# Performance work log

Hardware: AMD Instinct MI355X
Metric: run time of the kernel (lower is better)

Reference implementation:

```python
import jax, jax.numpy as jnp
import numpy as np

N_ENT = 50000
N_REL = 500
N_EDGE = 640000
D_IN = 128
D_OUT = 128
NEG_SLOPE = 0.01  # torch nn.LeakyReLU default
BN_EPS = 1e-5


def setup_inputs() -> dict:
    key = jax.random.key(0)
    ks = jax.random.split(key, 16)
    edge_index = jax.random.randint(ks[0], (2, N_EDGE), 0, N_ENT)
    edge_type = jax.random.randint(ks[1], (N_EDGE,), 0, N_REL)
    query_type = jax.random.randint(ks[2], (N_EDGE,), 0, N_REL)
    entity_embed = jax.random.normal(ks[3], (N_ENT, D_IN), jnp.float32)
    rel_embed = jax.random.normal(ks[4], (N_REL, D_IN), jnp.float32)
    s = 0.05
    return {
        "edge_index": edge_index,
        "edge_type": edge_type,
        "query_type": query_type,
        "entity_embed": entity_embed,
        "rel_embed": rel_embed,
        "w_loop": jax.random.normal(ks[5], (D_IN, D_OUT), jnp.float32) * s,
        "w_out": jax.random.normal(ks[6], (D_IN, D_OUT), jnp.float32) * s,
        "w_rel": jax.random.normal(ks[7], (D_IN, D_OUT), jnp.float32) * s,
        "loop_rel": jax.random.normal(ks[8], (1, D_IN), jnp.float32) * s,
        "W_w": jax.random.normal(ks[9], (D_IN, D_IN), jnp.float32) * s,   # W.weight^T layout: x @ W_w
        "W_b": jnp.zeros((D_IN,), jnp.float32),
        "a_w": jax.random.normal(ks[10], (2 * D_IN, 1), jnp.float32) * s,
        "a_b": jnp.zeros((1,), jnp.float32),
        "bias": jnp.zeros((D_OUT,), jnp.float32),
        "bn_gamma": jnp.ones((D_OUT,), jnp.float32),
        "bn_beta": jnp.zeros((D_OUT,), jnp.float32),
    }


def _compgcn_fwd(edge_index, edge_type, query_type, entity_embed, rel_embed,
                 w_loop, w_out, w_rel, loop_rel, W_w, W_b, a_w, a_b,
                 bias, bn_gamma, bn_beta):
    N = entity_embed.shape[0]
    rel_all = jnp.concatenate([rel_embed, loop_rel], axis=0)  # (R+1, D)
    row, col = edge_index[0], edge_index[1]  # values already in [0, N)

    # edge norm: 1/out-degree of source node (deg[row] >= 1 for every edge)
    deg = jax.ops.segment_sum(jnp.ones((row.shape[0],), entity_embed.dtype), row, num_segments=N)
    norm = 1.0 / deg[row]  # (E,)

    # self-loop branch (mode='loop'): rel_transform 'mult' with loop relation, no attention
    loop_res = (entity_embed * rel_all[-1]) @ w_loop  # (N, D_out)

    # out branch (mode='out')
    x_j = entity_embed[col]          # (E, D)
    r_e = rel_all[edge_type]         # (E, D)
    q_e = rel_all[query_type]        # (E, D)
    xj_rel = x_j * r_e               # 'mult' composition

    h = jnp.concatenate([r_e @ W_w + W_b, q_e @ W_w + W_b], axis=-1)  # (E, 2D)
    logits = h @ a_w + a_b                                            # (E, 1)
    alpha = jnp.exp(jax.nn.leaky_relu(logits[:, 0], NEG_SLOPE))       # (E,)
    sum_alpha = jax.ops.segment_sum(alpha, row, num_segments=N)       # (N,)
    alpha = alpha / sum_alpha[row]

    msg = (xj_rel @ w_out) * (alpha * norm)[:, None]                  # (E, D_out)
    out_res = jax.ops.segment_sum(msg, row, num_segments=N)           # (N, D_out)

    out = 0.5 * out_res + 0.5 * loop_res + bias  # dropout = identity (eval)
    # BatchNorm1d, training-mode batch statistics (biased var), over node dim
    mean = jnp.mean(out, axis=0)
    var = jnp.mean((out - mean) ** 2, axis=0)
    out = (out - mean) * jax.lax.rsqrt(var + BN_EPS) * bn_gamma + bn_beta

    ent_out = jax.nn.leaky_relu(out, NEG_SLOPE)
    rel_out = (rel_all @ w_rel)[:-1]
    return ent_out, rel_out


def reference(edge_index, edge_type, query_type, entity_embed, rel_embed,
              w_loop, w_out, w_rel, loop_rel, W_w, W_b, a_w, a_b,
              bias, bn_gamma, bn_beta):
    return _compgcn_fwd(edge_index, edge_type, query_type, entity_embed, rel_embed,
                        w_loop, w_out, w_rel, loop_rel, W_w, W_b, a_w, a_b,
                        bias, bn_gamma, bn_beta)
```

## Files before the change

### kernel.cpp

```cpp
#include <hip/hip_runtime.h>
#include <math.h>

#define E_N 640000
#define N_N 50000
#define R_N 500
#define D   128
#define NEG 0.01f
#define BNEPS 1e-5f
#define CAP 48

typedef __bf16 bf16x8 __attribute__((ext_vector_type(8)));
typedef float f32x4 __attribute__((ext_vector_type(4)));

#define CNT_OFF    0u
#define STAT_OFF   50000u
#define ZERO_FLOATS 50256u
#define BUCKET_OFF 50256u
#define ENTBF_OFF  4850256u
#define RELBF_OFF  8050256u
#define BT_OFF     8082256u
#define S1_OFF     8098640u
#define S2_OFF     8099152u

__device__ __forceinline__ float lrelu(float x) { return x > 0.f ? x : NEG * x; }

__device__ __forceinline__ void st_bf16x4(__bf16* p, float x, float y, float z, float w) {
    union { __bf16 b[4]; uint2 u; } pk;
    pk.b[0] = (__bf16)x; pk.b[1] = (__bf16)y; pk.b[2] = (__bf16)z; pk.b[3] = (__bf16)w;
    *(uint2*)p = pk.u;
}

__device__ __forceinline__ void st_bf16x8(__bf16* p, const float* v) {
    union { __bf16 b[8]; uint4 u; } pk;
#pragma unroll
    for (int j = 0; j < 8; ++j) pk.b[j] = (__bf16)v[j];
    *(uint4*)p = pk.u;
}

__device__ __forceinline__ void fma8(uint4 ue, uint4 ur, float a, float* acc) {
    const unsigned* we = (const unsigned*)&ue;
    const unsigned* wr = (const unsigned*)&ur;
#pragma unroll
    for (int w = 0; w < 4; ++w) {
        float e_lo = __uint_as_float(we[w] << 16);
        float e_hi = __uint_as_float(we[w] & 0xffff0000u);
        float r_lo = __uint_as_float(wr[w] << 16);
        float r_hi = __uint_as_float(wr[w] & 0xffff0000u);
        acc[2 * w]     = fmaf(a * e_lo, r_lo, acc[2 * w]);
        acc[2 * w + 1] = fmaf(a * e_hi, r_hi, acc[2 * w + 1]);
    }
}

#define P1_S   501
#define P1_WB  256
#define P1_REL 500

__global__ __launch_bounds__(128) void k_pre1(const float* __restrict__ Ww,
                                              const float* __restrict__ Wb,
                                              const float* __restrict__ aw,
                                              const float* __restrict__ rel,
                                              const float* __restrict__ looprel,
                                              const float* __restrict__ wout,
                                              const float* __restrict__ wloop,
                                              const float* __restrict__ wrel,
                                              float* __restrict__ s1,
                                              float* __restrict__ s2,
                                              __bf16* __restrict__ Bt,
                                              float* __restrict__ out_rel,
                                              __bf16* __restrict__ rel_bf) {
    int b = blockIdx.x, t = threadIdx.x;
    if (b < P1_S) {
        __shared__ float rr[D];
        __shared__ float part[4];
        const float* rp = (b < R_N) ? rel + (size_t)b * D : looprel;
        rr[t] = rp[t];
        if (b < R_N) rel_bf[(size_t)b * D + t] = (__bf16)rp[t];
        __syncthreads();
        float v = 0.f;
        for (int i = 0; i < D; ++i) v = fmaf(rr[i], Ww[i * D + t], v);
        float p1 = aw[t] * v + Wb[t] * aw[t];
        float p2 = aw[D + t] * v + Wb[t] * aw[D + t];
        for (int o = 32; o; o >>= 1) {
            p1 += __shfl_down(p1, o);
            p2 += __shfl_down(p2, o);
        }
        if ((t & 63) == 0) {
            part[(t >> 6) * 2] = p1;
            part[(t >> 6) * 2 + 1] = p2;
        }
        __syncthreads();
        if (t == 0) {
            s1[b] = part[0] + part[2];
            s2[b] = part[1] + part[3];
        }
    } else if (b < P1_S + P1_WB) {
        int idx = (b - P1_S) * 128 + t;
        int n = idx & 127, k = idx >> 7;
        float v = (k < D) ? wout[(size_t)k * D + n] : wloop[(size_t)(k - D) * D + n];
        Bt[(size_t)n * 256 + k] = (__bf16)v;
    } else {
        int r = b - (P1_S + P1_WB);
        __shared__ float rr2[D];
        rr2[t] = rel[(size_t)r * D + t];
        __syncthreads();
        float a = 0.f;
        for (int k = 0; k < D; ++k) a = fmaf(rr2[k], wrel[(size_t)k * D + t], a);
        out_rel[(size_t)r * D + t] = a;
    }
}

#define P2_BIN 625
#define P2_ENT 1563

__global__ __launch_bounds__(256) void k_pre2(const int* __restrict__ row,
                                              const int* __restrict__ col,
                                              const int* __restrict__ et,
                                              const int* __restrict__ qt,
                                              const float* __restrict__ s1,
                                              const float* __restrict__ s2,
                                              const float* __restrict__ ab,
                                              const float* __restrict__ ent,
                                              int* __restrict__ cnt,
                                              int2* __restrict__ bucket,
                                              __bf16* __restrict__ ent_bf) {
    int b = blockIdx.x, t = threadIdx.x;
    if (b < P2_BIN) {
        int e0 = b * 1024 + t;
        int r[4], c[4], te[4];
        float a[4];
#pragma unroll
        for (int j = 0; j < 4; ++j) {
            int e = e0 + j * 256;
            r[j] = row[e];
            c[j] = col[e];
            te[j] = et[e];
            int q = qt[e];
            a[j] = __expf(lrelu(s1[te[j]] + s2[q] + ab[0]));
        }
        int pos[4];
#pragma unroll
        for (int j = 0; j < 4; ++j) pos[j] = atomicAdd(&cnt[r[j]], 1);
#pragma unroll
        for (int j = 0; j < 4; ++j) {
            if (pos[j] < CAP) {
                bucket[(size_t)r[j] * CAP + pos[j]] =
                    make_int2(c[j] | (te[j] << 16), __float_as_int(a[j]));
            }
        }
    } else {
        int blk = b - P2_BIN;
        const float4* e4 = (const float4*)ent;
#pragma unroll
        for (int j = 0; j < 4; ++j) {
            int idx = blk * 1024 + j * 256 + t;
            if (idx < N_N * D / 4) {
                float4 v = e4[idx];
                st_bf16x4(ent_bf + (size_t)idx * 4, v.x, v.y, v.z, v.w);
            }
        }
    }
}

__global__ __launch_bounds__(128) void k_gather(const int* __restrict__ cnt,
                                                const int2* __restrict__ bucket,
                                                const __bf16* __restrict__ ent_bf,
                                                const __bf16* __restrict__ rel_bf,
                                                const float* __restrict__ looprel,
                                                __bf16* __restrict__ stage) {
    int n = blockIdx.x, t = threadIdx.x;
    int deg = cnt[n];
    int m = deg < CAP ? deg : CAP;
    __shared__ int eoff[CAP];
    __shared__ int roff[CAP];
    __shared__ float sa[CAP];
    __shared__ float xred[16][8];
    if (t < CAP) {
        if (t < m) {
            int2 be = bucket[(size_t)n * CAP + t];
            eoff[t] = (be.x & 0xffff) << 8;
            roff[t] = (be.x >> 16) << 8;
            sa[t] = __int_as_float(be.y);
        } else {
            eoff[t] = 0; roff[t] = 0; sa[t] = 0.f;
        }
    }
    __syncthreads();
    float suma = 0.f;
    for (int i = 0; i < m; ++i) suma += sa[i];
    int s = t & 15, g = t >> 4;
    const char* eb = (const char*)ent_bf;
    const char* rb = (const char*)rel_bf;
    int co = s * 16;
    float acc[8] = {0, 0, 0, 0, 0, 0, 0, 0};
#define EDGE(e_) { \
        uint4 ue = *(const uint4*)(eb + (eoff[e_] + co)); \
        uint4 ur = *(const uint4*)(rb + (roff[e_] + co)); \
        fma8(ue, ur, sa[e_], acc); }
    EDGE(g) EDGE(g + 8)
    if (m > 16) { EDGE(g + 16) EDGE(g + 24) }
    if (m > 32) { EDGE(g + 32) EDGE(g + 40) }
#undef EDGE
#pragma unroll
    for (int k = 0; k < 8; ++k) {
        acc[k] += __shfl_xor(acc[k], 16);
        acc[k] += __shfl_xor(acc[k], 32);
    }
    if (t >= 64 && t < 80) {
#pragma unroll
        for (int k = 0; k < 8; ++k) xred[s][k] = acc[k];
    }
    if (t >= 96 && t < 112) {
        int si = t - 96;
        uint4 ue = *(const uint4*)(eb + ((size_t)n << 8) + si * 16);
        const unsigned* we = (const unsigned*)&ue;
        float v[8];
#pragma unroll
        for (int w = 0; w < 4; ++w) {
            v[2 * w]     = __uint_as_float(we[w] << 16) * looprel[si * 8 + 2 * w];
            v[2 * w + 1] = __uint_as_float(we[w] & 0xffff0000u) * looprel[si * 8 + 2 * w + 1];
        }
        st_bf16x8(stage + (size_t)n * 256 + 128 + si * 8, v);
    }
    __syncthreads();
    if (t < 16) {
        float inv = (deg > 0) ? 1.0f / (suma * (float)deg) : 0.f;
        float v[8];
#pragma unroll
        for (int k = 0; k < 8; ++k) v[k] = (acc[k] + xred[s][k]) * inv;
        st_bf16x8(stage + (size_t)n * 256 + s * 8, v);
    }
}

__global__ __launch_bounds__(256) void k_gemm(const __bf16* stage,
                                              const __bf16* __restrict__ Bt,
                                              const float* __restrict__ bias,
                                              float* out,
                                              float* __restrict__ stat) {
    int t = threadIdx.x;
    int wave = t >> 6, l = t & 63;
    int lm = l & 15, lg = l >> 4;
    size_t mbase = (size_t)blockIdx.x * 128 + wave * 32;
    const bf16x8* A = (const bf16x8*)stage;
    const bf16x8* B = (const bf16x8*)Bt;
    f32x4 acc[2][8];
#pragma unroll
    for (int mt = 0; mt < 2; ++mt)
#pragma unroll
        for (int nt = 0; nt < 8; ++nt) acc[mt][nt] = (f32x4)(0.f);
#pragma unroll
    for (int ks = 0; ks < 8; ++ks) {
        bf16x8 a0 = A[(mbase + lm) * 32 + ks * 4 + lg];
        bf16x8 a1 = A[(mbase + 16 + lm) * 32 + ks * 4 + lg];
#pragma unroll
        for (int nt = 0; nt < 8; ++nt) {
            bf16x8 b = B[(size_t)(nt * 16 + lm) * 32 + ks * 4 + lg];
            acc[0][nt] = __builtin_amdgcn_mfma_f32_16x16x32_bf16(a0, b, acc[0][nt], 0, 0, 0);
            acc[1][nt] = __builtin_amdgcn_mfma_f32_16x16x32_bf16(a1, b, acc[1][nt], 0, 0, 0);
        }
    }
    float psum[8], psq[8];
#pragma unroll
    for (int nt = 0; nt < 8; ++nt) { psum[nt] = 0.f; psq[nt] = 0.f; }
#pragma unroll
    for (int mt = 0; mt < 2; ++mt) {
#pragma unroll
        for (int nt = 0; nt < 8; ++nt) {
            int c = nt * 16 + lm;
            float bv = bias[c];
#pragma unroll
            for (int r = 0; r < 4; ++r) {
                size_t rowi = mbase + mt * 16 + lg * 4 + r;
                if (rowi < N_N) {
                    float v = 0.5f * acc[mt][nt][r] + bv;
                    out[rowi * D + c] = v;
                    psum[nt] += v;
                    psq[nt] += v * v;
                }
            }
        }
    }
    __shared__ float2 red[8][16][16];
    int slot = wave * 4 + lg;
#pragma unroll
    for (int nt = 0; nt < 8; ++nt) red[nt][lm][slot] = make_float2(psum[nt], psq[nt]);
    __syncthreads();
    if (t < 128) {
        int nt = t >> 4, lmm = t & 15;
        float ss = 0.f, qq = 0.f;
#pragma unroll
        for (int k = 0; k < 16; ++k) {
            float2 v = red[nt][lmm][k];
            ss += v.x;
            qq += v.y;
        }
        atomicAdd(&stat[t], ss);
        atomicAdd(&stat[D + t], qq);
    }
}

__global__ __launch_bounds__(256) void k_bnapply(float* __restrict__ out,
                                                 const float* __restrict__ stat,
                                                 const float* __restrict__ gamma,
                                                 const float* __restrict__ beta) {
    __shared__ float ssc[D], ssh[D];
    int t = threadIdx.x;
    if (t < D) {
        float mean = stat[t] * (1.0f / N_N);
        float var = stat[D + t] * (1.0f / N_N) - mean * mean;
        float sc = gamma[t] * rsqrtf(var + BNEPS);
        ssc[t] = sc;
        ssh[t] = beta[t] - mean * sc;
    }
    __syncthreads();
    const float4* sc4 = (const float4*)ssc;
    const float4* sh4 = (const float4*)ssh;
    float4* o4 = (float4*)out;
    const int total = N_N * D / 4;
    for (int i = blockIdx.x * blockDim.x + t; i < total; i += gridDim.x * blockDim.x) {
        int d4 = i & 31;
        float4 v = o4[i];
        float4 s = sc4[d4];
        float4 h = sh4[d4];
        v.x = lrelu(v.x * s.x + h.x);
        v.y = lrelu(v.y * s.y + h.y);
        v.z = lrelu(v.z * s.z + h.z);
        v.w = lrelu(v.w * s.w + h.w);
        o4[i] = v;
    }
}

extern "C" void kernel_launch(void* const* d_in, const int* in_sizes, int n_in,
                              void* d_out, int out_size, void* d_ws, size_t ws_size,
                              hipStream_t stream) {
    const int* edge_index = (const int*)d_in[0];
    const int* row = edge_index;
    const int* col = edge_index + E_N;
    const int* etype = (const int*)d_in[1];
    const int* qtype = (const int*)d_in[2];
    const float* ent = (const float*)d_in[3];
    const float* rel = (const float*)d_in[4];
    const float* w_loop = (const float*)d_in[5];
    const float* w_out = (const float*)d_in[6];
    const float* w_rel = (const float*)d_in[7];
    const float* loop_rel = (const float*)d_in[8];
    const float* W_w = (const float*)d_in[9];
    const float* W_b = (const float*)d_in[10];
    const float* a_w = (const float*)d_in[11];
    const float* a_b = (const float*)d_in[12];
    const float* bias = (const float*)d_in[13];
    const float* bn_gamma = (const float*)d_in[14];
    const float* bn_beta = (const float*)d_in[15];

    float* ws = (float*)d_ws;
    int* cnt = (int*)(ws + CNT_OFF);
    float* stat = ws + STAT_OFF;
    int2* bucket = (int2*)(ws + BUCKET_OFF);
    __bf16* ent_bf = (__bf16*)(ws + ENTBF_OFF);
    __bf16* rel_bf = (__bf16*)(ws + RELBF_OFF);
    __bf16* Bt = (__bf16*)(ws + BT_OFF);
    float* s1 = ws + S1_OFF;
    float* s2 = ws + S2_OFF;

    float* out_ent = (float*)d_out;
    float* out_rel = out_ent + (size_t)N_N * D;
    __bf16* stage = (__bf16*)d_out;

    hipMemsetAsync(d_ws, 0, (size_t)ZERO_FLOATS * sizeof(float), stream);

    k_pre1<<<P1_S + P1_WB + P1_REL, 128, 0, stream>>>(
        W_w, W_b, a_w, rel, loop_rel, w_out, w_loop, w_rel,
        s1, s2, Bt, out_rel, rel_bf);
    k_pre2<<<P2_BIN + P2_ENT, 256, 0, stream>>>(
        row, col, etype, qtype, s1, s2, a_b, ent, cnt, bucket, ent_bf);
    k_gather<<<N_N, 128, 0, stream>>>(cnt, bucket, ent_bf, rel_bf, loop_rel, stage);
    k_gemm<<<(N_N + 127) / 128, 256, 0, stream>>>(stage, Bt, bias, out_ent, stat);
    k_bnapply<<<2048, 256, 0, stream>>>(out_ent, stat, bn_gamma, bn_beta);
}
```

Baseline: 144.4 us.

## Partition edge binning by row range to localize atomics and bucket writes

Edge binning is split into 8 row-range groups. Consecutive blocks each read the same edge chunk, but a block only inserts edges whose source row falls in its group, so concurrent atomics and bucket writes land in a compact address range that should sit better in each XCD's L2. The gather kernel maps block IDs in the same interleaved way. The entity bf16 conversion moves into k_pre1. The cost is that every block rereads the full row array, giving 8x the row reads.

```diff
diff --git a/kernel.cpp b/kernel.cpp
--- a/kernel.cpp
+++ b/kernel.cpp
@@ -8,6 +8,8 @@
 #define NEG 0.01f
 #define BNEPS 1e-5f
 #define CAP 48
+#define GROUPS 8
+#define RPG 6250
 
 typedef __bf16 bf16x8 __attribute__((ext_vector_type(8)));
 typedef float f32x4 __attribute__((ext_vector_type(4)));
@@ -54,6 +56,7 @@
 #define P1_S   501
 #define P1_WB  256
 #define P1_REL 500
+#define P1_ENT 1563
 
 __global__ __launch_bounds__(128) void k_pre1(const float* __restrict__ Ww,
                                               const float* __restrict__ Wb,
@@ -63,11 +66,13 @@
                                               const float* __restrict__ wout,
                                               const float* __restrict__ wloop,
                                               const float* __restrict__ wrel,
+                                              const float* __restrict__ ent,
                                               float* __restrict__ s1,
                                               float* __restrict__ s2,
                                               __bf16* __restrict__ Bt,
                                               float* __restrict__ out_rel,
-                                              __bf16* __restrict__ rel_bf) {
+                                              __bf16* __restrict__ rel_bf,
+                                              __bf16* __restrict__ ent_bf) {
     int b = blockIdx.x, t = threadIdx.x;
     if (b < P1_S) {
         __shared__ float rr[D];
@@ -98,7 +103,7 @@
         int n = idx & 127, k = idx >> 7;
         float v = (k < D) ? wout[(size_t)k * D + n] : wloop[(size_t)(k - D) * D + n];
         Bt[(size_t)n * 256 + k] = (__bf16)v;
-    } else {
+    } else if (b < P1_S + P1_WB + P1_REL) {
         int r = b - (P1_S + P1_WB);
         __shared__ float rr2[D];
         rr2[t] = rel[(size_t)r * D + t];
@@ -106,56 +111,50 @@
         float a = 0.f;
         for (int k = 0; k < D; ++k) a = fmaf(rr2[k], wrel[(size_t)k * D + t], a);
         out_rel[(size_t)r * D + t] = a;
-    }
-}
-
-#define P2_BIN 625
-#define P2_ENT 1563
-
-__global__ __launch_bounds__(256) void k_pre2(const int* __restrict__ row,
-                                              const int* __restrict__ col,
-                                              const int* __restrict__ et,
-                                              const int* __restrict__ qt,
-                                              const float* __restrict__ s1,
-                                              const float* __restrict__ s2,
-                                              const float* __restrict__ ab,
-                                              const float* __restrict__ ent,
-                                              int* __restrict__ cnt,
-                                              int2* __restrict__ bucket,
-                                              __bf16* __restrict__ ent_bf) {
-    int b = blockIdx.x, t = threadIdx.x;
-    if (b < P2_BIN) {
-        int e0 = b * 1024 + t;
-        int r[4], c[4], te[4];
-        float a[4];
-#pragma unroll
-        for (int j = 0; j < 4; ++j) {
-            int e = e0 + j * 256;
-            r[j] = row[e];
-            c[j] = col[e];
-            te[j] = et[e];
-            int q = qt[e];
-            a[j] = __expf(lrelu(s1[te[j]] + s2[q] + ab[0]));
-        }
-        int pos[4];
-#pragma unroll
-        for (int j = 0; j < 4; ++j) pos[j] = atomicAdd(&cnt[r[j]], 1);
-#pragma unroll
-        for (int j = 0; j < 4; ++j) {
-            if (pos[j] < CAP) {
-                bucket[(size_t)r[j] * CAP + pos[j]] =
-                    make_int2(c[j] | (te[j] << 16), __float_as_int(a[j]));
-            }
-        }
     } else {
-        int blk = b - P2_BIN;
+        int blk = b - (P1_S + P1_WB + P1_REL);
         const float4* e4 = (const float4*)ent;
 #pragma unroll
-        for (int j = 0; j < 4; ++j) {
-            int idx = blk * 1024 + j * 256 + t;
+        for (int j = 0; j < 8; ++j) {
+            int idx = blk * 1024 + j * 128 + t;
             if (idx < N_N * D / 4) {
                 float4 v = e4[idx];
                 st_bf16x4(ent_bf + (size_t)idx * 4, v.x, v.y, v.z, v.w);
+            }
+        }
+    }
+}
+
+#define BIN_BLOCKS (625 * GROUPS)
+
+__global__ __launch_bounds__(256) void k_bin(const int* __restrict__ row,
+                                             const int* __restrict__ col,
+                                             const int* __restrict__ et,
+                                             const int* __restrict__ qt,
+                                             const float* __restrict__ s1,
+                                             const float* __restrict__ s2,
+                                             const float* __restrict__ ab,
+                                             int* __restrict__ cnt,
+                                             int2* __restrict__ bucket) {
+    int b = blockIdx.x, t = threadIdx.x;
+    int g = b & 7;
+    int chunk = b >> 3;
+    int rlo = g * RPG;
+    int e0 = chunk * 1024 + t;
+    int r[4];
+#pragma unroll
+    for (int j = 0; j < 4; ++j) r[j] = row[e0 + j * 256];
+#pragma unroll
+    for (int j = 0; j < 4; ++j) {
+        unsigned rr = (unsigned)(r[j] - rlo);
+        if (rr < RPG) {
+            int e = e0 + j * 256;
+            int c = col[e], te = et[e], q = qt[e];
+            float a = __expf(lrelu(s1[te] + s2[q] + ab[0]));
+            int pos = atomicAdd(&cnt[r[j]], 1);
+            if (pos < CAP) {
+                bucket[(size_t)r[j] * CAP + pos] =
+                    make_int2(c | (te << 16), __float_as_int(a));
             }
         }
     }
@@ -167,7 +166,8 @@
                                                 const __bf16* __restrict__ rel_bf,
                                                 const float* __restrict__ looprel,
                                                 __bf16* __restrict__ stage) {
-    int n = blockIdx.x, t = threadIdx.x;
+    int n = (blockIdx.x & 7) * RPG + (blockIdx.x >> 3);
+    int t = threadIdx.x;
     int deg = cnt[n];
     int m = deg < CAP ? deg : CAP;
     __shared__ int eoff[CAP];
@@ -367,11 +367,11 @@
 
     hipMemsetAsync(d_ws, 0, (size_t)ZERO_FLOATS * sizeof(float), stream);
 
-    k_pre1<<<P1_S + P1_WB + P1_REL, 128, 0, stream>>>(
-        W_w, W_b, a_w, rel, loop_rel, w_out, w_loop, w_rel,
-        s1, s2, Bt, out_rel, rel_bf);
-    k_pre2<<<P2_BIN + P2_ENT, 256, 0, stream>>>(
-        row, col, etype, qtype, s1, s2, a_b, ent, cnt, bucket, ent_bf);
+    k_pre1<<<P1_S + P1_WB + P1_REL + P1_ENT, 128, 0, stream>>>(
+        W_w, W_b, a_w, rel, loop_rel, w_out, w_loop, w_rel, ent,
+        s1, s2, Bt, out_rel, rel_bf, ent_bf);
+    k_bin<<<BIN_BLOCKS, 256, 0, stream>>>(
+        row, col, etype, qtype, s1, s2, a_b, cnt, bucket);
     k_gather<<<N_N, 128, 0, stream>>>(cnt, bucket, ent_bf, rel_bf, loop_rel, stage);
     k_gemm<<<(N_N + 127) / 128, 256, 0, stream>>>(stage, Bt, bias, out_ent, stat);
     k_bnapply<<<2048, 256, 0, stream>>>(out_ent, stat, bn_gamma, bn_beta);
```

New measurement: 136.5 us. 5.5% less time.
